# Optimization experiments

Measured on AMD Instinct MI355X. Metric: run time of the kernel, lower is better.

The kernel has to match this reference:

```python
import jax, jax.numpy as jnp
import numpy as np

DIM = 1024
HEADS = 16
SCALE = DIM ** -0.5  # NOTE: original scales by full dim, not head dim


def setup_inputs() -> dict:
    key = jax.random.key(0)
    ks = jax.random.split(key, 6)
    B, S, D = 2, 2048, DIM
    x = jax.random.normal(ks[0], (B, S, D), dtype=jnp.float32)
    Wq = jax.random.normal(ks[1], (D, D), dtype=jnp.float32) * 0.02
    Wk = jax.random.normal(ks[2], (D, D), dtype=jnp.float32) * 0.02
    Wv = jax.random.normal(ks[3], (D, D), dtype=jnp.float32) * 0.02
    Wo = jax.random.normal(ks[4], (D, D), dtype=jnp.float32) * 0.02
    z = jnp.zeros((D,), dtype=jnp.float32)
    return {"x": x, "Wq": Wq, "bq": z, "Wk": Wk, "bk": z, "Wv": Wv, "bv": z, "Wo": Wo, "bo": z}


def reference(x, Wq, bq, Wk, bk, Wv, bv, Wo, bo):
    B, S, D = x.shape
    H = HEADS
    d = D // H
    # projections (Linear: x @ W + b)
    q = (x @ Wq + bq).reshape(B, S, H, d).transpose(0, 2, 1, 3)  # b h i d
    k = (x @ Wk + bk).reshape(B, S, H, d).transpose(0, 2, 1, 3)  # b h j d
    v = (x @ Wv + bv).reshape(B, S, H, d).transpose(0, 2, 1, 3)  # b h j d
    dots = jnp.einsum("bhid,bhjd->bhij", q, k) * SCALE
    # causal mask: strict upper triangle -> -inf
    mask = jnp.triu(jnp.ones((S, S), dtype=bool), k=1)
    dots = jnp.where(mask, -jnp.inf, dots)
    attn = jax.nn.softmax(dots, axis=-1)
    out = jnp.einsum("bhij,bhjd->bhid", attn, v)
    out = out.transpose(0, 2, 1, 3).reshape(B, S, D)  # b i (h d)
    return out @ Wo + bo
```

## Files before the change

kernel.cpp:

```cpp
#include <hip/hip_runtime.h>
#include <hip/hip_bf16.h>

typedef __bf16 bf16;
typedef __bf16 bf16x4 __attribute__((ext_vector_type(4)));
typedef __bf16 bf16x8 __attribute__((ext_vector_type(8)));
typedef float floatx4 __attribute__((ext_vector_type(4)));

#define MFMA_16x16x32(a, b, c) __builtin_amdgcn_mfma_f32_16x16x32_bf16((a), (b), (c), 0, 0, 0)
#define NEG_INF (-__builtin_inff())

#define CB 2
#define CS 2048
#define CD 1024
#define CH 16
#define CM (CB * CS)
#define QSC (0.03125f * 1.44269504088896340736f)

__device__ __forceinline__ void async16(const bf16* g, bf16* l) {
    __builtin_amdgcn_global_load_lds(
        (const __attribute__((address_space(1))) void*)g,
        (__attribute__((address_space(3))) void*)l, 16, 0, 0);
}

__global__ __launch_bounds__(256) void conv_x(const float* __restrict__ x,
                                              bf16* __restrict__ xb) {
    size_t i = ((size_t)blockIdx.x * 256 + threadIdx.x) * 8;
    float4 a = *(const float4*)(x + i);
    float4 b = *(const float4*)(x + i + 4);
    bf16x8 v;
    v[0] = (bf16)a.x; v[1] = (bf16)a.y; v[2] = (bf16)a.z; v[3] = (bf16)a.w;
    v[4] = (bf16)b.x; v[5] = (bf16)b.y; v[6] = (bf16)b.z; v[7] = (bf16)b.w;
    *(bf16x8*)(xb + i) = v;
}

__global__ __launch_bounds__(256) void conv_wt(
    const float* __restrict__ W0, const float* __restrict__ W1,
    const float* __restrict__ W2, const float* __restrict__ W3,
    bf16* __restrict__ Wt) {
    __shared__ bf16 Ws[64 * 68];
    const float* W = blockIdx.z == 0 ? W0 : blockIdx.z == 1 ? W1
                   : blockIdx.z == 2 ? W2 : W3;
    bf16* out = Wt + (size_t)blockIdx.z * CD * CD;
    const int t = threadIdx.x;
    const int n0 = blockIdx.x * 64, k0 = blockIdx.y * 64;
    const int rr = t >> 4, c4 = (t & 15) * 4;
#pragma unroll
    for (int i = 0; i < 4; i++) {
        int r = rr + i * 16;
        float4 f = *(const float4*)(W + (size_t)(k0 + r) * CD + n0 + c4);
        bf16x4 v;
        v[0] = (bf16)f.x; v[1] = (bf16)f.y; v[2] = (bf16)f.z; v[3] = (bf16)f.w;
        *(bf16x4*)&Ws[r * 68 + c4] = v;
    }
    __syncthreads();
#pragma unroll
    for (int i = 0; i < 4; i++) {
        int n = rr + i * 16;
        bf16x4 v;
#pragma unroll
        for (int j = 0; j < 4; j++) v[j] = Ws[(c4 + j) * 68 + n];
        *(bf16x4*)(out + (size_t)(n0 + n) * CD + k0 + c4) = v;
    }
}

__global__ __launch_bounds__(256) void gemm_qkv(
    const bf16* __restrict__ A, const bf16* __restrict__ Bt,
    const float* __restrict__ bq, const float* __restrict__ bk,
    const float* __restrict__ bv,
    bf16* __restrict__ Qb, bf16* __restrict__ Kb, bf16* __restrict__ Vb) {
    __shared__ bf16 As[128 * 32];
    __shared__ bf16 Bs[128 * 32];
    const int t = threadIdx.x, w = t >> 6, lane = t & 63;
    const int quad = lane >> 4, l15 = lane & 15;
    const int which = blockIdx.x >> 3;
    const int bn = (blockIdx.x & 7) * 128, bm = blockIdx.y * 128;
    const bf16* Bw = Bt + (size_t)which * CD * CD;

    const bf16* ag = A + (size_t)(bm + w * 16 + (lane >> 2)) * CD + (lane & 3) * 8;
    const bf16* bg = Bw + (size_t)(bn + w * 16 + (lane >> 2)) * CD + (lane & 3) * 8;
    const int lo = w * 16 * 32;

    const int wm = (w >> 1) * 64, wn = (w & 1) * 64;
    floatx4 acc[4][4] = {};

    for (int k0 = 0; k0 < CD; k0 += 32) {
        async16(ag + k0, &As[lo]);
        async16(ag + (size_t)64 * CD + k0, &As[lo + 64 * 32]);
        async16(bg + k0, &Bs[lo]);
        async16(bg + (size_t)64 * CD + k0, &Bs[lo + 64 * 32]);
        __syncthreads();
        bf16x8 af[4], bfr[4];
#pragma unroll
        for (int mt = 0; mt < 4; mt++)
            af[mt] = *(const bf16x8*)&As[(wm + mt * 16 + l15) * 32 + quad * 8];
#pragma unroll
        for (int nt = 0; nt < 4; nt++)
            bfr[nt] = *(const bf16x8*)&Bs[(wn + nt * 16 + l15) * 32 + quad * 8];
#pragma unroll
        for (int mt = 0; mt < 4; mt++)
#pragma unroll
            for (int nt = 0; nt < 4; nt++)
                acc[mt][nt] = MFMA_16x16x32(af[mt], bfr[nt], acc[mt][nt]);
        __syncthreads();
    }

    const float* bias = which == 0 ? bq : which == 1 ? bk : bv;
    bf16* out = which == 0 ? Qb : Kb;
#pragma unroll
    for (int mt = 0; mt < 4; mt++) {
#pragma unroll
        for (int nt = 0; nt < 4; nt++) {
            int token = bm + wm + mt * 16 + quad * 4;
            int col = bn + wn + nt * 16 + l15;
            int b = token >> 11, s = token & (CS - 1);
            int h = col >> 6, dd = col & 63;
            if (which == 2) {
                bf16x4 pv;
#pragma unroll
                for (int r = 0; r < 4; r++) pv[r] = (bf16)(acc[mt][nt][r] + bias[col]);
                *(bf16x4*)&Vb[(((size_t)(b * CH + h)) * 64 + dd) * CS + s] = pv;
            } else {
#pragma unroll
                for (int r = 0; r < 4; r++) {
                    float v = acc[mt][nt][r] + bias[col];
                    if (which == 0) v *= QSC;
                    out[(((size_t)(b * CH + h)) * CS + s + r) * 64 + dd] = (bf16)v;
                }
            }
        }
    }
}

__global__ __launch_bounds__(256) void gemm_o(
    const bf16* __restrict__ A, const bf16* __restrict__ Bt,
    const float* __restrict__ bias, float* __restrict__ out) {
    __shared__ bf16 As[64 * 32];
    __shared__ bf16 Bs[128 * 32];
    const int t = threadIdx.x, w = t >> 6, lane = t & 63;
    const int quad = lane >> 4, l15 = lane & 15;
    const int bn = blockIdx.x * 128, bm = blockIdx.y * 64;

    const bf16* ag = A + (size_t)(bm + w * 16 + (lane >> 2)) * CD + (lane & 3) * 8;
    const bf16* bg = Bt + (size_t)(bn + w * 16 + (lane >> 2)) * CD + (lane & 3) * 8;
    const int lo = w * 16 * 32;

    const int wm = (w >> 1) * 32, wn = (w & 1) * 64;
    floatx4 acc[2][4] = {};

    for (int k0 = 0; k0 < CD; k0 += 32) {
        async16(ag + k0, &As[lo]);
        async16(bg + k0, &Bs[lo]);
        async16(bg + (size_t)64 * CD + k0, &Bs[lo + 64 * 32]);
        __syncthreads();
        bf16x8 af[2], bfr[4];
#pragma unroll
        for (int mt = 0; mt < 2; mt++)
            af[mt] = *(const bf16x8*)&As[(wm + mt * 16 + l15) * 32 + quad * 8];
#pragma unroll
        for (int nt = 0; nt < 4; nt++)
            bfr[nt] = *(const bf16x8*)&Bs[(wn + nt * 16 + l15) * 32 + quad * 8];
#pragma unroll
        for (int mt = 0; mt < 2; mt++)
#pragma unroll
            for (int nt = 0; nt < 4; nt++)
                acc[mt][nt] = MFMA_16x16x32(af[mt], bfr[nt], acc[mt][nt]);
        __syncthreads();
    }

#pragma unroll
    for (int mt = 0; mt < 2; mt++)
#pragma unroll
        for (int nt = 0; nt < 4; nt++)
#pragma unroll
            for (int r = 0; r < 4; r++) {
                int row = bm + wm + mt * 16 + quad * 4 + r;
                int col = bn + wn + nt * 16 + l15;
                out[(size_t)row * CD + col] = acc[mt][nt][r] + bias[col];
            }
}

__global__ __launch_bounds__(512) void attn_kernel(
    const bf16* __restrict__ Q, const bf16* __restrict__ Kg,
    const bf16* __restrict__ Vg, bf16* __restrict__ Ob) {
    __shared__ bf16 Ks[2][2][64 * 72];
    __shared__ bf16 Vt[2][2][64 * 72];
    __shared__ bf16 Pt[8][32 * 72];

    const int t = threadIdx.x;
    const int w = t >> 6, lane = t & 63;
    const int grp = w >> 2, wg = w & 3;
    const int quad = lane >> 4, l15 = lane & 15;

    const int qb = 15 - (blockIdx.x >> 5);
    const int bh = blockIdx.x & 31;
    const int q0 = qb * 128;
    const int wrow0 = q0 + wg * 32;
    const int nT = 2 * qb + 2;
    const int nS = nT >> 1;

    const bf16* Qh = Q + (size_t)bh * CS * 64;
    const bf16* Kh = Kg + (size_t)bh * CS * 64;
    const bf16* Vh = Vg + (size_t)bh * 64 * CS;

    const int tl = t & 255;
    const int strow = tl >> 2, soff = (tl & 3) * 16;
    const bf16* ksrc = Kh + (size_t)strow * 64 + soff;
    const bf16* vsrc = Vh + (size_t)strow * CS + soff;
    const int sbase = strow * 72 + soff;

    {
        const bf16* k0p = ksrc + (size_t)grp * 64 * 64;
        const bf16* v0p = vsrc + grp * 64;
        bf16x8 a = *(const bf16x8*)k0p, b = *(const bf16x8*)(k0p + 8);
        bf16x8 c = *(const bf16x8*)v0p, d = *(const bf16x8*)(v0p + 8);
        *(bf16x8*)&Ks[grp][0][sbase]     = a;
        *(bf16x8*)&Ks[grp][0][sbase + 8] = b;
        *(bf16x8*)&Vt[grp][0][sbase]     = c;
        *(bf16x8*)&Vt[grp][0][sbase + 8] = d;
    }
    bf16x8 kr0, kr1, vr0, vr1;
    {
        int t1 = (grp + 2 < nT) ? grp + 2 : 0;
        const bf16* kn = ksrc + (size_t)t1 * 64 * 64;
        const bf16* vn = vsrc + t1 * 64;
        kr0 = *(const bf16x8*)kn;  kr1 = *(const bf16x8*)(kn + 8);
        vr0 = *(const bf16x8*)vn;  vr1 = *(const bf16x8*)(vn + 8);
    }

    bf16x8 qf[2][2];
#pragma unroll
    for (int g = 0; g < 2; g++) {
        const bf16* qsrc = Qh + (size_t)(wrow0 + g * 16 + l15) * 64 + quad * 8;
        qf[g][0] = *(const bf16x8*)qsrc;
        qf[g][1] = *(const bf16x8*)(qsrc + 32);
    }

    floatx4 o[4][2] = {};
    float m_r[2] = {NEG_INF, NEG_INF};
    float l_r[2] = {0.f, 0.f};

    bf16* pw = Pt[w];

    for (int s = 0; s < nS; s++) {
        const int tile = 2 * s + grp;
        const int cur = s & 1;
        const int ks0 = tile * 64;
        __syncthreads();

        *(bf16x8*)&Ks[grp][cur ^ 1][sbase]     = kr0;
        *(bf16x8*)&Ks[grp][cur ^ 1][sbase + 8] = kr1;
        *(bf16x8*)&Vt[grp][cur ^ 1][sbase]     = vr0;
        *(bf16x8*)&Vt[grp][cur ^ 1][sbase + 8] = vr1;
        {
            int nk = (tile + 4 < nT) ? tile + 4 : 0;
            const bf16* kn = ksrc + (size_t)nk * 64 * 64;
            const bf16* vn = vsrc + nk * 64;
            kr0 = *(const bf16x8*)kn;  kr1 = *(const bf16x8*)(kn + 8);
            vr0 = *(const bf16x8*)vn;  vr1 = *(const bf16x8*)(vn + 8);
        }
        if (ks0 > wrow0 + 31) continue;

        const bf16* ksb = Ks[grp][cur];
        const bf16* vtb = Vt[grp][cur];

        floatx4 sc[2][4] = {};
        __builtin_amdgcn_s_setprio(1);
#pragma unroll
        for (int nt = 0; nt < 4; nt++) {
            bf16x8 af0 = *(const bf16x8*)&ksb[(nt * 16 + l15) * 72 + quad * 8];
            bf16x8 af1 = *(const bf16x8*)&ksb[(nt * 16 + l15) * 72 + 32 + quad * 8];
#pragma unroll
            for (int g = 0; g < 2; g++) {
                sc[g][nt] = MFMA_16x16x32(af0, qf[g][0], sc[g][nt]);
                sc[g][nt] = MFMA_16x16x32(af1, qf[g][1], sc[g][nt]);
            }
        }
        __builtin_amdgcn_s_setprio(0);
        if (ks0 + 63 > wrow0) {
#pragma unroll
            for (int g = 0; g < 2; g++) {
                int qrow = wrow0 + g * 16 + l15;
#pragma unroll
                for (int nt = 0; nt < 4; nt++)
#pragma unroll
                    for (int r = 0; r < 4; r++)
                        if (ks0 + nt * 16 + quad * 4 + r > qrow)
                            sc[g][nt][r] = NEG_INF;
            }
        }
        float mx[2];
#pragma unroll
        for (int g = 0; g < 2; g++) {
            floatx4 v01, v23, vm;
#pragma unroll
            for (int c = 0; c < 4; c++) {
                v01[c] = fmaxf(sc[g][0][c], sc[g][1][c]);
                v23[c] = fmaxf(sc[g][2][c], sc[g][3][c]);
                vm[c] = fmaxf(v01[c], v23[c]);
            }
            float m = fmaxf(fmaxf(vm[0], vm[1]), fmaxf(vm[2], vm[3]));
            m = fmaxf(m, __shfl_xor(m, 16));
            m = fmaxf(m, __shfl_xor(m, 32));
            mx[g] = m;
        }
        int need = (mx[0] > m_r[0] + 8.f) || (mx[1] > m_r[1] + 8.f);
        if (__any(need)) {
#pragma unroll
            for (int g = 0; g < 2; g++) {
                float mn = fmaxf(m_r[g], mx[g]);
                float a = __builtin_amdgcn_exp2f(m_r[g] - mn);
                m_r[g] = mn;
                l_r[g] *= a;
#pragma unroll
                for (int dt = 0; dt < 4; dt++)
#pragma unroll
                    for (int r = 0; r < 4; r++) o[dt][g][r] *= a;
            }
        }
#pragma unroll
        for (int g = 0; g < 2; g++) {
#pragma unroll
            for (int nt = 0; nt < 4; nt++)
#pragma unroll
                for (int r = 0; r < 4; r++)
                    sc[g][nt][r] = __builtin_amdgcn_exp2f(sc[g][nt][r] - m_r[g]);
            floatx4 st = (sc[g][0] + sc[g][1]) + (sc[g][2] + sc[g][3]);
            l_r[g] += (st[0] + st[1]) + (st[2] + st[3]);
        }
#pragma unroll
        for (int g = 0; g < 2; g++)
#pragma unroll
            for (int nt = 0; nt < 4; nt++) {
                bf16x4 pk;
#pragma unroll
                for (int r = 0; r < 4; r++) pk[r] = (bf16)sc[g][nt][r];
                *(bf16x4*)&pw[(g * 16 + l15) * 72 + nt * 16 + quad * 4] = pk;
            }
        bf16x8 bp[2][2];
#pragma unroll
        for (int g = 0; g < 2; g++) {
            bp[g][0] = *(const bf16x8*)&pw[(g * 16 + l15) * 72 + quad * 8];
            bp[g][1] = *(const bf16x8*)&pw[(g * 16 + l15) * 72 + 32 + quad * 8];
        }
        __builtin_amdgcn_s_setprio(1);
#pragma unroll
        for (int dt = 0; dt < 4; dt++) {
            bf16x8 av0 = *(const bf16x8*)&vtb[(dt * 16 + l15) * 72 + quad * 8];
            bf16x8 av1 = *(const bf16x8*)&vtb[(dt * 16 + l15) * 72 + 32 + quad * 8];
#pragma unroll
            for (int g = 0; g < 2; g++) {
                o[dt][g] = MFMA_16x16x32(av0, bp[g][0], o[dt][g]);
                o[dt][g] = MFMA_16x16x32(av1, bp[g][1], o[dt][g]);
            }
        }
        __builtin_amdgcn_s_setprio(0);
    }

    __syncthreads();
    float* mg = (float*)&Ks[0][0][0];
    float* base = mg + (size_t)(wg * 64 + lane) * 36;
    if (grp == 1) {
#pragma unroll
        for (int dt = 0; dt < 4; dt++)
#pragma unroll
            for (int g = 0; g < 2; g++)
                *(floatx4*)(base + (dt * 2 + g) * 4) = o[dt][g];
        base[32] = m_r[0]; base[33] = m_r[1];
        base[34] = l_r[0]; base[35] = l_r[1];
    }
    __syncthreads();
    if (grp == 0) {
        float a0[2], a1[2];
#pragma unroll
        for (int g = 0; g < 2; g++) {
            float m1 = base[32 + g], l1 = base[34 + g];
            float mm = fmaxf(m_r[g], m1);
            a0[g] = __builtin_amdgcn_exp2f(m_r[g] - mm);
            a1[g] = __builtin_amdgcn_exp2f(m1 - mm);
            l_r[g] = l_r[g] * a0[g] + l1 * a1[g];
        }
#pragma unroll
        for (int dt = 0; dt < 4; dt++)
#pragma unroll
            for (int g = 0; g < 2; g++) {
                floatx4 o1 = *(const floatx4*)(base + (dt * 2 + g) * 4);
#pragma unroll
                for (int r = 0; r < 4; r++)
                    o[dt][g][r] = o[dt][g][r] * a0[g] + o1[r] * a1[g];
            }
        const int b = bh >> 4, h = bh & 15;
#pragma unroll
        for (int g = 0; g < 2; g++) {
            float l = l_r[g];
            l += __shfl_xor(l, 16);
            l += __shfl_xor(l, 32);
            float rl = 1.f / l;
            int row = wrow0 + g * 16 + l15;
#pragma unroll
            for (int dt = 0; dt < 4; dt++) {
                bf16x4 ov;
#pragma unroll
                for (int r = 0; r < 4; r++) ov[r] = (bf16)(o[dt][g][r] * rl);
                *(bf16x4*)&Ob[((size_t)b * CS + row) * CD + h * 64 + dt * 16 + quad * 4] = ov;
            }
        }
    }
}

extern "C" void kernel_launch(void* const* d_in, const int* in_sizes, int n_in,
                              void* d_out, int out_size, void* d_ws, size_t ws_size,
                              hipStream_t stream) {
    const float* x  = (const float*)d_in[0];
    const float* Wq = (const float*)d_in[1];
    const float* bq = (const float*)d_in[2];
    const float* Wk = (const float*)d_in[3];
    const float* bk = (const float*)d_in[4];
    const float* Wv = (const float*)d_in[5];
    const float* bv = (const float*)d_in[6];
    const float* Wo = (const float*)d_in[7];
    const float* bo = (const float*)d_in[8];
    float* out = (float*)d_out;

    bf16* xb = (bf16*)d_ws;
    bf16* Wt = xb + (size_t)CM * CD;
    bf16* Qb = Wt + (size_t)4 * CD * CD;
    bf16* Kb = Qb + (size_t)CB * CH * CS * 64;
    bf16* Vb = Kb + (size_t)CB * CH * CS * 64;
    bf16* Ob = Vb + (size_t)CB * CH * CS * 64;

    conv_x<<<(CM * CD) / (256 * 8), 256, 0, stream>>>(x, xb);
    conv_wt<<<dim3(CD / 64, CD / 64, 4), 256, 0, stream>>>(Wq, Wk, Wv, Wo, Wt);

    gemm_qkv<<<dim3(24, CM / 128), 256, 0, stream>>>(
        xb, Wt, bq, bk, bv, Qb, Kb, Vb);

    attn_kernel<<<512, 512, 0, stream>>>(Qb, Kb, Vb, Ob);

    gemm_o<<<dim3(8, CM / 64), 256, 0, stream>>>(
        Ob, Wt + (size_t)3 * CD * CD, bo, out);
}
```

Before: 181.8 us.

## Fuse conversion kernels, enlarge output GEMM tile, single-buffer attention LDS for occupancy

The two fp32-to-bf16 conversion kernels are merged into one launch, which removes a kernel launch. The output projection GEMM tile grows from 64x128 to 128x128, so fewer blocks each do more MFMA work per LDS load. The attention kernel drops its double-buffered K/V shared memory for a single buffer with an extra barrier, and adds a launch-bounds hint that targets higher occupancy. Its block order also changes so that heavy and light causal query blocks are interleaved. The trade-off is an extra synchronization per iteration in attention and half as many gemm_o blocks (256) for the device's CUs.

```diff
diff --git a/kernel.cpp b/kernel.cpp
--- a/kernel.cpp
+++ b/kernel.cpp
@@ -22,27 +22,28 @@
         (__attribute__((address_space(3))) void*)l, 16, 0, 0);
 }
 
-__global__ __launch_bounds__(256) void conv_x(const float* __restrict__ x,
-                                              bf16* __restrict__ xb) {
-    size_t i = ((size_t)blockIdx.x * 256 + threadIdx.x) * 8;
-    float4 a = *(const float4*)(x + i);
-    float4 b = *(const float4*)(x + i + 4);
-    bf16x8 v;
-    v[0] = (bf16)a.x; v[1] = (bf16)a.y; v[2] = (bf16)a.z; v[3] = (bf16)a.w;
-    v[4] = (bf16)b.x; v[5] = (bf16)b.y; v[6] = (bf16)b.z; v[7] = (bf16)b.w;
-    *(bf16x8*)(xb + i) = v;
-}
-
-__global__ __launch_bounds__(256) void conv_wt(
+__global__ __launch_bounds__(256) void prep(
+    const float* __restrict__ x, bf16* __restrict__ xb,
     const float* __restrict__ W0, const float* __restrict__ W1,
     const float* __restrict__ W2, const float* __restrict__ W3,
     bf16* __restrict__ Wt) {
     __shared__ bf16 Ws[64 * 68];
-    const float* W = blockIdx.z == 0 ? W0 : blockIdx.z == 1 ? W1
-                   : blockIdx.z == 2 ? W2 : W3;
-    bf16* out = Wt + (size_t)blockIdx.z * CD * CD;
     const int t = threadIdx.x;
-    const int n0 = blockIdx.x * 64, k0 = blockIdx.y * 64;
+    if (blockIdx.x < 2048) {
+        size_t i = ((size_t)blockIdx.x * 256 + t) * 8;
+        float4 a = *(const float4*)(x + i);
+        float4 b = *(const float4*)(x + i + 4);
+        bf16x8 v;
+        v[0] = (bf16)a.x; v[1] = (bf16)a.y; v[2] = (bf16)a.z; v[3] = (bf16)a.w;
+        v[4] = (bf16)b.x; v[5] = (bf16)b.y; v[6] = (bf16)b.z; v[7] = (bf16)b.w;
+        *(bf16x8*)(xb + i) = v;
+        return;
+    }
+    const int bid = blockIdx.x - 2048;
+    const int z = bid >> 8, rem = bid & 255;
+    const int k0 = (rem >> 4) * 64, n0 = (rem & 15) * 64;
+    const float* W = z == 0 ? W0 : z == 1 ? W1 : z == 2 ? W2 : W3;
+    bf16* out = Wt + (size_t)z * CD * CD;
     const int rr = t >> 4, c4 = (t & 15) * 4;
 #pragma unroll
     for (int i = 0; i < 4; i++) {
@@ -134,33 +135,34 @@
 __global__ __launch_bounds__(256) void gemm_o(
     const bf16* __restrict__ A, const bf16* __restrict__ Bt,
     const float* __restrict__ bias, float* __restrict__ out) {
-    __shared__ bf16 As[64 * 32];
+    __shared__ bf16 As[128 * 32];
     __shared__ bf16 Bs[128 * 32];
     const int t = threadIdx.x, w = t >> 6, lane = t & 63;
     const int quad = lane >> 4, l15 = lane & 15;
-    const int bn = blockIdx.x * 128, bm = blockIdx.y * 64;
+    const int bn = blockIdx.x * 128, bm = blockIdx.y * 128;
 
     const bf16* ag = A + (size_t)(bm + w * 16 + (lane >> 2)) * CD + (lane & 3) * 8;
     const bf16* bg = Bt + (size_t)(bn + w * 16 + (lane >> 2)) * CD + (lane & 3) * 8;
     const int lo = w * 16 * 32;
 
-    const int wm = (w >> 1) * 32, wn = (w & 1) * 64;
-    floatx4 acc[2][4] = {};
+    const int wm = (w >> 1) * 64, wn = (w & 1) * 64;
+    floatx4 acc[4][4] = {};
 
     for (int k0 = 0; k0 < CD; k0 += 32) {
         async16(ag + k0, &As[lo]);
+        async16(ag + (size_t)64 * CD + k0, &As[lo + 64 * 32]);
         async16(bg + k0, &Bs[lo]);
         async16(bg + (size_t)64 * CD + k0, &Bs[lo + 64 * 32]);
         __syncthreads();
-        bf16x8 af[2], bfr[4];
-#pragma unroll
-        for (int mt = 0; mt < 2; mt++)
+        bf16x8 af[4], bfr[4];
+#pragma unroll
+        for (int mt = 0; mt < 4; mt++)
             af[mt] = *(const bf16x8*)&As[(wm + mt * 16 + l15) * 32 + quad * 8];
 #pragma unroll
         for (int nt = 0; nt < 4; nt++)
             bfr[nt] = *(const bf16x8*)&Bs[(wn + nt * 16 + l15) * 32 + quad * 8];
 #pragma unroll
-        for (int mt = 0; mt < 2; mt++)
+        for (int mt = 0; mt < 4; mt++)
 #pragma unroll
             for (int nt = 0; nt < 4; nt++)
                 acc[mt][nt] = MFMA_16x16x32(af[mt], bfr[nt], acc[mt][nt]);
@@ -168,7 +170,7 @@
     }
 
 #pragma unroll
-    for (int mt = 0; mt < 2; mt++)
+    for (int mt = 0; mt < 4; mt++)
 #pragma unroll
         for (int nt = 0; nt < 4; nt++)
 #pragma unroll
@@ -179,11 +181,11 @@
             }
 }
 
-__global__ __launch_bounds__(512) void attn_kernel(
+__global__ __launch_bounds__(512, 4) void attn_kernel(
     const bf16* __restrict__ Q, const bf16* __restrict__ Kg,
     const bf16* __restrict__ Vg, bf16* __restrict__ Ob) {
-    __shared__ bf16 Ks[2][2][64 * 72];
-    __shared__ bf16 Vt[2][2][64 * 72];
+    __shared__ bf16 Ks[2][64 * 72];
+    __shared__ bf16 Vt[2][64 * 72];
     __shared__ bf16 Pt[8][32 * 72];
 
     const int t = threadIdx.x;
@@ -191,8 +193,9 @@
     const int grp = w >> 2, wg = w & 3;
     const int quad = lane >> 4, l15 = lane & 15;
 
-    const int qb = 15 - (blockIdx.x >> 5);
-    const int bh = blockIdx.x & 31;
+    const int bid = blockIdx.x;
+    const int qb = bid < 256 ? 15 - (bid >> 5) : (bid - 256) >> 5;
+    const int bh = bid & 31;
     const int q0 = qb * 128;
     const int wrow0 = q0 + wg * 32;
     const int nT = 2 * qb + 2;
@@ -208,21 +211,10 @@
     const bf16* vsrc = Vh + (size_t)strow * CS + soff;
     const int sbase = strow * 72 + soff;
 
-    {
-        const bf16* k0p = ksrc + (size_t)grp * 64 * 64;
-        const bf16* v0p = vsrc + grp * 64;
-        bf16x8 a = *(const bf16x8*)k0p, b = *(const bf16x8*)(k0p + 8);
-        bf16x8 c = *(const bf16x8*)v0p, d = *(const bf16x8*)(v0p + 8);
-        *(bf16x8*)&Ks[grp][0][sbase]     = a;
-        *(bf16x8*)&Ks[grp][0][sbase + 8] = b;
-        *(bf16x8*)&Vt[grp][0][sbase]     = c;
-        *(bf16x8*)&Vt[grp][0][sbase + 8] = d;
-    }
     bf16x8 kr0, kr1, vr0, vr1;
     {
-        int t1 = (grp + 2 < nT) ? grp + 2 : 0;
-        const bf16* kn = ksrc + (size_t)t1 * 64 * 64;
-        const bf16* vn = vsrc + t1 * 64;
+        const bf16* kn = ksrc + (size_t)grp * 64 * 64;
+        const bf16* vn = vsrc + grp * 64;
         kr0 = *(const bf16x8*)kn;  kr1 = *(const bf16x8*)(kn + 8);
         vr0 = *(const bf16x8*)vn;  vr1 = *(const bf16x8*)(vn + 8);
     }
@@ -243,25 +235,24 @@
 
     for (int s = 0; s < nS; s++) {
         const int tile = 2 * s + grp;
-        const int cur = s & 1;
         const int ks0 = tile * 64;
         __syncthreads();
-
-        *(bf16x8*)&Ks[grp][cur ^ 1][sbase]     = kr0;
-        *(bf16x8*)&Ks[grp][cur ^ 1][sbase + 8] = kr1;
-        *(bf16x8*)&Vt[grp][cur ^ 1][sbase]     = vr0;
-        *(bf16x8*)&Vt[grp][cur ^ 1][sbase + 8] = vr1;
+        *(bf16x8*)&Ks[grp][sbase]     = kr0;
+        *(bf16x8*)&Ks[grp][sbase + 8] = kr1;
+        *(bf16x8*)&Vt[grp][sbase]     = vr0;
+        *(bf16x8*)&Vt[grp][sbase + 8] = vr1;
         {
-            int nk = (tile + 4 < nT) ? tile + 4 : 0;
+            int nk = (tile + 2 < nT) ? tile + 2 : 0;
             const bf16* kn = ksrc + (size_t)nk * 64 * 64;
             const bf16* vn = vsrc + nk * 64;
             kr0 = *(const bf16x8*)kn;  kr1 = *(const bf16x8*)(kn + 8);
             vr0 = *(const bf16x8*)vn;  vr1 = *(const bf16x8*)(vn + 8);
         }
+        __syncthreads();
         if (ks0 > wrow0 + 31) continue;
 
-        const bf16* ksb = Ks[grp][cur];
-        const bf16* vtb = Vt[grp][cur];
+        const bf16* ksb = Ks[grp];
+        const bf16* vtb = Vt[grp];
 
         floatx4 sc[2][4] = {};
         __builtin_amdgcn_s_setprio(1);
@@ -357,7 +348,7 @@
     }
 
     __syncthreads();
-    float* mg = (float*)&Ks[0][0][0];
+    float* mg = (float*)&Pt[0][0];
     float* base = mg + (size_t)(wg * 64 + lane) * 36;
     if (grp == 1) {
 #pragma unroll
@@ -428,14 +419,13 @@
     bf16* Vb = Kb + (size_t)CB * CH * CS * 64;
     bf16* Ob = Vb + (size_t)CB * CH * CS * 64;
 
-    conv_x<<<(CM * CD) / (256 * 8), 256, 0, stream>>>(x, xb);
-    conv_wt<<<dim3(CD / 64, CD / 64, 4), 256, 0, stream>>>(Wq, Wk, Wv, Wo, Wt);
+    prep<<<3072, 256, 0, stream>>>(x, xb, Wq, Wk, Wv, Wo, Wt);
 
     gemm_qkv<<<dim3(24, CM / 128), 256, 0, stream>>>(
         xb, Wt, bq, bk, bv, Qb, Kb, Vb);
 
     attn_kernel<<<512, 512, 0, stream>>>(Qb, Kb, Vb, Ob);
 
-    gemm_o<<<dim3(8, CM / 64), 256, 0, stream>>>(
+    gemm_o<<<dim3(8, CM / 128), 256, 0, stream>>>(
         Ob, Wt + (size_t)3 * CD * CD, bo, out);
 }
```

After: 196.9 us. 8.3% more time.
